# Kernel optimization log

Measured on AMD Instinct MI355X. Metric: run time of the kernel, lower is better.

## Reference

```python
import jax, jax.numpy as jnp
import numpy as np
import math

B, S, E, H = 4, 2048, 1024, 16
D = E // H
NEG_INF = -1e30  # stands in for -inf in masked_fill; softmax result identical for rows with valid entries


def setup_inputs() -> dict:
    key = jax.random.key(0)
    ks = jax.random.split(key, 7)
    sc = 1.0 / math.sqrt(E)
    return {
        "k": jax.random.normal(ks[0], (B, S, E), jnp.float32),
        "v": jax.random.normal(ks[1], (B, S, E), jnp.float32),
        "q": jax.random.normal(ks[2], (B, S, E), jnp.float32),
        "Wk": jax.random.normal(ks[3], (E, E), jnp.float32) * sc,
        "Wv": jax.random.normal(ks[4], (E, E), jnp.float32) * sc,
        "Wq": jax.random.normal(ks[5], (E, E), jnp.float32) * sc,
        "Wo": jax.random.normal(ks[6], (E, E), jnp.float32) * sc,
    }


def reference(k, v, q, Wk, Wv, Wq, Wo):
    # Linear(bias=False): y = x @ W.T
    kp = (k @ Wk.T).reshape(B, S, H, D).transpose(0, 2, 1, 3)  # [B,H,S,D]
    vp = (v @ Wv.T).reshape(B, S, H, D).transpose(0, 2, 1, 3)
    qp = (q @ Wq.T).reshape(B, S, H, D).transpose(0, 2, 1, 3)
    qp = qp / jnp.sqrt(jnp.asarray(D, qp.dtype))
    scores = jnp.einsum("bhqd,bhkd->bhqk", qp, kp)  # [B,H,S,S]
    causal = jnp.tril(jnp.ones((S, S), bool))  # [S,S]
    scores = jnp.where(causal[None, None], scores, NEG_INF)
    attn = jax.nn.softmax(scores, axis=-1)  # dropout p=0.0 (eval) -> identity
    out = jnp.einsum("bhqk,bhkd->bhqd", attn, vp)
    out = out.transpose(0, 2, 1, 3).reshape(B, S, E)
    return out @ Wo.T
```

## Files before the change

### kernel.cpp

```cpp
#include <hip/hip_runtime.h>

typedef __bf16 bf16_t;
typedef __bf16 bf16x8 __attribute__((ext_vector_type(8)));
typedef float f32x4 __attribute__((ext_vector_type(4)));
typedef float f32x16 __attribute__((ext_vector_type(16)));


__device__ __forceinline__ void async_copy16(const void* g, void* l) {
  __builtin_amdgcn_global_load_lds(
      (const __attribute__((address_space(1))) void*)g,
      (__attribute__((address_space(3))) void*)l, 16, 0, 0);
}

__device__ __forceinline__ unsigned pk_bf16(float lo, float hi) {
  unsigned r;
  asm("v_cvt_pk_bf16_f32 %0, %1, %2" : "=v"(r) : "v"(lo), "v"(hi));
  return r;
}

__global__ void cvt_all_kernel(const float* __restrict__ q, const float* __restrict__ k,
                               const float* __restrict__ v, const float* __restrict__ wk,
                               const float* __restrict__ wv, const float* __restrict__ wq,
                               const float* __restrict__ wo, uint2* __restrict__ out) {
  constexpr int QX = 2097152, QW = 262144;
  int g = blockIdx.x * 256 + threadIdx.x;
  const float* in; int off;
  if (g < QX)               { in = q;  off = 0; }
  else if (g < 2 * QX)      { in = k;  off = QX; }
  else if (g < 3 * QX)      { in = v;  off = 2 * QX; }
  else if (g < 3 * QX + QW)     { in = wk; off = 3 * QX; }
  else if (g < 3 * QX + 2 * QW) { in = wv; off = 3 * QX + QW; }
  else if (g < 3 * QX + 3 * QW) { in = wq; off = 3 * QX + 2 * QW; }
  else                          { in = wo; off = 3 * QX + 3 * QW; }
  float4 val = ((const float4*)in)[g - off];
  union { bf16_t h[4]; uint2 u; } cv;
  cv.h[0] = (bf16_t)val.x; cv.h[1] = (bf16_t)val.y;
  cv.h[2] = (bf16_t)val.z; cv.h[3] = (bf16_t)val.w;
  out[g] = cv.u;
}

__global__ __launch_bounds__(256) void qkv_kernel(
    const bf16_t* __restrict__ qb, const bf16_t* __restrict__ kb, const bf16_t* __restrict__ vb,
    const bf16_t* __restrict__ wqb, const bf16_t* __restrict__ wkb, const bf16_t* __restrict__ wvb,
    bf16_t* __restrict__ Qp, bf16_t* __restrict__ Kp, bf16_t* __restrict__ Vt, float qscale)
{
  constexpr int K = 1024;
  __shared__ __align__(16) bf16_t As[128 * 32];
  __shared__ __align__(16) bf16_t Bs[128 * 32];
  const int tid  = threadIdx.x;
  const int lane = tid & 63;
  const int wid  = tid >> 6;
  const int quad = lane >> 4;
  const int l16  = lane & 15;
  const int bx = blockIdx.x, by = blockIdx.y;
  const int sel = by >> 3, sub = by & 7;
  const bf16_t *X, *W; bf16_t* Y; float scale = 1.0f;
  int m0, n0;
  if (sel == 0)      { X = qb;  W = wqb; Y = Qp; m0 = bx * 128; n0 = sub * 128; scale = qscale; }
  else if (sel == 1) { X = kb;  W = wkb; Y = Kp; m0 = bx * 128; n0 = sub * 128; }
  else               { X = wvb; W = vb;  Y = Vt; m0 = sub * 128; n0 = bx * 128; }
  const int wm = (wid >> 1) * 64;
  const int wn = (wid & 1) * 64;
  const int swz = quad ^ ((l16 >> 1) & 3);

  f32x4 acc[4][4] = {};

  for (int k0 = 0; k0 < K; k0 += 32) {
#pragma unroll
    for (int p = 0; p < 2; ++p) {
      int c = tid + p * 256;
      int row = c >> 2;
      int seg = ((c & 3) ^ ((c >> 3) & 3)) * 8;
      async_copy16(&X[(size_t)(m0 + row) * K + k0 + seg], (char*)As + (p * 256 + wid * 64) * 16);
      async_copy16(&W[(size_t)(n0 + row) * K + k0 + seg], (char*)Bs + (p * 256 + wid * 64) * 16);
    }
    __syncthreads();
    bf16x8 af[4], bfr[4];
#pragma unroll
    for (int i = 0; i < 4; ++i)
      af[i] = *(const bf16x8*)((const char*)As + ((wm + i * 16 + l16) * 4 + swz) * 16);
#pragma unroll
    for (int j = 0; j < 4; ++j)
      bfr[j] = *(const bf16x8*)((const char*)Bs + ((wn + j * 16 + l16) * 4 + swz) * 16);
#pragma unroll
    for (int i = 0; i < 4; ++i)
#pragma unroll
      for (int j = 0; j < 4; ++j)
        acc[i][j] = __builtin_amdgcn_mfma_f32_16x16x32_bf16(af[i], bfr[j], acc[i][j], 0, 0, 0);
    __syncthreads();
  }

#pragma unroll
  for (int i = 0; i < 4; ++i)
#pragma unroll
    for (int j = 0; j < 4; ++j)
#pragma unroll
      for (int r = 0; r < 4; ++r) {
        int row = m0 + wm + i * 16 + quad * 4 + r;
        int col = n0 + wn + j * 16 + l16;
        float val = acc[i][j][r] * scale;
        if (sel < 2) {
          int b = row >> 11, s = row & 2047;
          int h = col >> 6,  d = col & 63;
          Y[(((size_t)(b * 16 + h) << 11) + s) * 64 + d] = (bf16_t)val;
        } else {
          int h = row >> 6,  d = row & 63;
          int b = col >> 11, s = col & 2047;
          Y[(((size_t)((b * 16 + h) * 64 + d)) << 11) + s] = (bf16_t)val;
        }
      }
}

__global__ __launch_bounds__(256) void out_gemm_kernel(
    const bf16_t* __restrict__ X, const bf16_t* __restrict__ W,
    float* __restrict__ Y, int M, int N, int K)
{
  __shared__ __align__(16) bf16_t As[128 * 32];
  __shared__ __align__(16) bf16_t Bs[128 * 32];
  const int tid  = threadIdx.x;
  const int lane = tid & 63;
  const int wid  = tid >> 6;
  const int quad = lane >> 4;
  const int l16  = lane & 15;
  const int m0 = blockIdx.x * 128;
  const int n0 = blockIdx.y * 128;
  const int wm = (wid >> 1) * 64;
  const int wn = (wid & 1) * 64;
  const int swz = quad ^ ((l16 >> 1) & 3);

  f32x4 acc[4][4] = {};

  for (int k0 = 0; k0 < K; k0 += 32) {
#pragma unroll
    for (int p = 0; p < 2; ++p) {
      int c = tid + p * 256;
      int row = c >> 2;
      int seg = ((c & 3) ^ ((c >> 3) & 3)) * 8;
      async_copy16(&X[(size_t)(m0 + row) * K + k0 + seg], (char*)As + (p * 256 + wid * 64) * 16);
      async_copy16(&W[(size_t)(n0 + row) * K + k0 + seg], (char*)Bs + (p * 256 + wid * 64) * 16);
    }
    __syncthreads();
    bf16x8 af[4], bfr[4];
#pragma unroll
    for (int i = 0; i < 4; ++i)
      af[i] = *(const bf16x8*)((const char*)As + ((wm + i * 16 + l16) * 4 + swz) * 16);
#pragma unroll
    for (int j = 0; j < 4; ++j)
      bfr[j] = *(const bf16x8*)((const char*)Bs + ((wn + j * 16 + l16) * 4 + swz) * 16);
#pragma unroll
    for (int i = 0; i < 4; ++i)
#pragma unroll
      for (int j = 0; j < 4; ++j)
        acc[i][j] = __builtin_amdgcn_mfma_f32_16x16x32_bf16(af[i], bfr[j], acc[i][j], 0, 0, 0);
    __syncthreads();
  }

#pragma unroll
  for (int i = 0; i < 4; ++i)
#pragma unroll
    for (int j = 0; j < 4; ++j)
#pragma unroll
      for (int r = 0; r < 4; ++r) {
        int row = m0 + wm + i * 16 + quad * 4 + r;
        int col = n0 + wn + j * 16 + l16;
        Y[(size_t)row * N + col] = acc[i][j][r];
      }
}

__global__ __launch_bounds__(256, 3) void attn_kernel(
    const bf16_t* __restrict__ Qp, const bf16_t* __restrict__ Kp,
    const bf16_t* __restrict__ Vt, bf16_t* __restrict__ O,
    float* __restrict__ Oacc, float* __restrict__ Racc)
{
  constexpr int S = 2048, D = 64, E = 1024;
  constexpr int BQ = 128, BK = 64;
  __shared__ __align__(16) bf16_t Ks[3][8 * 64 * 8];
  __shared__ __align__(16) bf16_t Vs[2][8 * 64 * 8];
  float* rsbuf = (float*)Ks;

  const int tid = threadIdx.x, lane = tid & 63, wid = tid >> 6;
  const int l31 = lane & 31, hi = lane >> 5;

  const signed char QT_TAB[24] = {15,15,7,14,14,13,13,6,12,12,11,11,5,10,10,9,9,4,8,8,3,2,1,0};
  const signed char HF_TAB[24] = {0,1,2,0,1,0,1,2,0,1,0,1,2,0,1,0,1,2,0,1,2,2,2,2};
  const int rank = (int)blockIdx.x >> 6;
  const int bh   = (int)blockIdx.x & 63;
  const int b = bh >> 4, h = bh & 15;
  const int qt = QT_TAB[rank];
  const int hf = HF_TAB[rank];
  const int nks = 2 * qt + 2;
  int s0, s1, half; bool direct;
  if (hf == 2) { s0 = 0; s1 = nks; half = 0; direct = true; }
  else         { half = hf; s0 = half ? nks / 2 : 0; s1 = half ? nks : nks / 2; direct = false; }

  const int q0 = qt * BQ;
  const size_t base  = (size_t)bh * S * D;
  const size_t baseV = (size_t)bh * D * S;
  const int qmin = q0 + wid * 32;
  const int qmax = qmin + 31;

  bf16x8 qf[4];
#pragma unroll
  for (int ks = 0; ks < 4; ++ks)
    qf[ks] = *(const bf16x8*)&Qp[base + (size_t)(qmin + l31) * D + ks * 16 + hi * 8];

  auto stageK = [&](int kt, int buf) {
#pragma unroll
    for (int is = 0; is < 2; ++is) {
      const int c = is * 256 + tid;
      const int p = c >> 6, row = c & 63;
      async_copy16(&Kp[base + (size_t)(kt * BK + row) * D + p * 8],
                   (char*)Ks[buf] + (is * 256 + wid * 64) * 16);
    }
  };
  auto stageV = [&](int kt, int buf) {
#pragma unroll
    for (int is = 0; is < 2; ++is) {
      const int c = is * 256 + tid;
      const int p = c >> 6, row = c & 63;
      async_copy16(&Vt[baseV + (size_t)row * S + kt * BK + p * 8],
                   (char*)Vs[buf] + (is * 256 + wid * 64) * 16);
    }
  };

  stageK(s0, s0 % 3);
  stageV(s0, s0 & 1);
  if (s0 + 1 < s1) stageK(s0 + 1, (s0 + 1) % 3);

  const f32x16 z16 = {};
  f32x16 oa0 = {}, oa1 = {};
  float rs = 0.0f;

  for (int kt = s0; kt < s1; ++kt) {
    const int k0 = kt * BK;
    const bool live = (k0 <= qmax);
    if (kt + 1 < s1) { asm volatile("s_waitcnt vmcnt(4)" ::: "memory"); }
    else             { asm volatile("s_waitcnt vmcnt(2)" ::: "memory"); }
    __builtin_amdgcn_s_barrier();
    __builtin_amdgcn_sched_barrier(0);
    if (kt + 1 < s1) stageV(kt + 1, (kt + 1) & 1);
    if (kt + 2 < s1) stageK(kt + 2, (kt + 2) % 3);

    unsigned pw[16];
    if (live) {
      const bf16_t* ksb = Ks[kt % 3];
      f32x16 sc0, sc1;
      {
        const bf16x8 kf0 = *(const bf16x8*)&ksb[(hi * 64 + l31) * 8];
        const bf16x8 kf1 = *(const bf16x8*)&ksb[(hi * 64 + 32 + l31) * 8];
        sc0 = __builtin_amdgcn_mfma_f32_32x32x16_bf16(kf0, qf[0], z16, 0, 0, 0);
        sc1 = __builtin_amdgcn_mfma_f32_32x32x16_bf16(kf1, qf[0], z16, 0, 0, 0);
      }
#pragma unroll
      for (int ks = 1; ks < 4; ++ks) {
        const bf16x8 kf0 = *(const bf16x8*)&ksb[((ks * 2 + hi) * 64 + l31) * 8];
        const bf16x8 kf1 = *(const bf16x8*)&ksb[((ks * 2 + hi) * 64 + 32 + l31) * 8];
        sc0 = __builtin_amdgcn_mfma_f32_32x32x16_bf16(kf0, qf[ks], sc0, 0, 0, 0);
        sc1 = __builtin_amdgcn_mfma_f32_32x32x16_bf16(kf1, qf[ks], sc1, 0, 0, 0);
      }
      if (k0 + 63 > qmin) {
        const int qg = qmin + l31;
#pragma unroll
        for (int r = 0; r < 16; ++r) {
          const int kg = k0 + (r & 3) + 8 * (r >> 2) + 4 * hi;
          if (kg > qg)      sc0[r] = -1e30f;
          if (kg + 32 > qg) sc1[r] = -1e30f;
        }
      }
#pragma unroll
      for (int r = 0; r < 16; ++r) {
        sc0[r] = __builtin_amdgcn_exp2f(sc0[r]);
        sc1[r] = __builtin_amdgcn_exp2f(sc1[r]);
      }
      {
        float s0a = 0.f, s1a = 0.f, s2a = 0.f, s3a = 0.f;
#pragma unroll
        for (int r = 0; r < 16; r += 4) {
          s0a += sc0[r]     + sc1[r];
          s1a += sc0[r + 1] + sc1[r + 1];
          s2a += sc0[r + 2] + sc1[r + 2];
          s3a += sc0[r + 3] + sc1[r + 3];
        }
        rs += (s0a + s1a) + (s2a + s3a);
      }
      {
        unsigned a0 = pk_bf16(sc0[0], sc0[1]),   a1 = pk_bf16(sc0[2], sc0[3]);
        unsigned b0 = pk_bf16(sc0[4], sc0[5]),   b1 = pk_bf16(sc0[6], sc0[7]);
        unsigned c0 = pk_bf16(sc0[8], sc0[9]),   c1 = pk_bf16(sc0[10], sc0[11]);
        unsigned d0 = pk_bf16(sc0[12], sc0[13]), d1 = pk_bf16(sc0[14], sc0[15]);
        asm("v_permlane32_swap_b32 %0, %1" : "+v"(a0), "+v"(b0));
        asm("v_permlane32_swap_b32 %0, %1" : "+v"(a1), "+v"(b1));
        asm("v_permlane32_swap_b32 %0, %1" : "+v"(c0), "+v"(d0));
        asm("v_permlane32_swap_b32 %0, %1" : "+v"(c1), "+v"(d1));
        pw[0] = a0; pw[1] = a1; pw[2] = b0; pw[3] = b1;
        pw[4] = c0; pw[5] = c1; pw[6] = d0; pw[7] = d1;
      }
      {
        unsigned a0 = pk_bf16(sc1[0], sc1[1]),   a1 = pk_bf16(sc1[2], sc1[3]);
        unsigned b0 = pk_bf16(sc1[4], sc1[5]),   b1 = pk_bf16(sc1[6], sc1[7]);
        unsigned c0 = pk_bf16(sc1[8], sc1[9]),   c1 = pk_bf16(sc1[10], sc1[11]);
        unsigned d0 = pk_bf16(sc1[12], sc1[13]), d1 = pk_bf16(sc1[14], sc1[15]);
        asm("v_permlane32_swap_b32 %0, %1" : "+v"(a0), "+v"(b0));
        asm("v_permlane32_swap_b32 %0, %1" : "+v"(a1), "+v"(b1));
        asm("v_permlane32_swap_b32 %0, %1" : "+v"(c0), "+v"(d0));
        asm("v_permlane32_swap_b32 %0, %1" : "+v"(c1), "+v"(d1));
        pw[8]  = a0; pw[9]  = a1; pw[10] = b0; pw[11] = b1;
        pw[12] = c0; pw[13] = c1; pw[14] = d0; pw[15] = d1;
      }
    }
    if (kt + 2 < s1)      { asm volatile("s_waitcnt vmcnt(6)" ::: "memory"); }
    else if (kt + 1 < s1) { asm volatile("s_waitcnt vmcnt(4)" ::: "memory"); }
    else                  { asm volatile("s_waitcnt vmcnt(0)" ::: "memory"); }
    __builtin_amdgcn_s_barrier();
    __builtin_amdgcn_sched_barrier(0);
    if (live) {
      const bf16_t* vsb = Vs[kt & 1];
      union U8 { unsigned u[4]; bf16x8 v; };
#pragma unroll
      for (int kb = 0; kb < 2; ++kb)
#pragma unroll
        for (int ks2 = 0; ks2 < 2; ++ks2) {
          U8 pu;
          pu.u[0] = pw[kb * 8 + ks2 * 4 + 0];
          pu.u[1] = pw[kb * 8 + ks2 * 4 + 1];
          pu.u[2] = pw[kb * 8 + ks2 * 4 + 2];
          pu.u[3] = pw[kb * 8 + ks2 * 4 + 3];
          const int pnl = kb * 4 + ks2 * 2 + hi;
          const bf16x8 vf0 = *(const bf16x8*)&vsb[(pnl * 64 + l31) * 8];
          const bf16x8 vf1 = *(const bf16x8*)&vsb[(pnl * 64 + 32 + l31) * 8];
          oa0 = __builtin_amdgcn_mfma_f32_32x32x16_bf16(pu.v, vf0, oa0, 0, 0, 0);
          oa1 = __builtin_amdgcn_mfma_f32_32x32x16_bf16(pu.v, vf1, oa1, 0, 0, 0);
        }
    }
  }

  const float full = rs + __shfl(rs, lane ^ 32);
  if (direct) {
    __syncthreads();
    if (lane < 32) rsbuf[wid * 32 + l31] = full;
    __syncthreads();
#pragma unroll
    for (int r = 0; r < 16; ++r) {
      const int crow = (r & 3) + 8 * (r >> 2) + 4 * hi;
      const float inv = __builtin_amdgcn_rcpf(rsbuf[wid * 32 + crow]);
      const int row = q0 + wid * 32 + crow;
      const size_t rowoff = ((size_t)(b * S + row)) * E + h * D;
      O[rowoff + l31]      = (bf16_t)(oa0[r] * inv);
      O[rowoff + 32 + l31] = (bf16_t)(oa1[r] * inv);
    }
  } else {
    float* Oh = Oacc + (size_t)half * (64 * 1024 * 64);
    float* Rh = Racc + (size_t)half * (64 * 1024);
    if (lane < 32) Rh[(size_t)bh * 1024 + (qmin + l31 - 1024)] = full;
#pragma unroll
    for (int r = 0; r < 16; ++r) {
      const int crow = (r & 3) + 8 * (r >> 2) + 4 * hi;
      const int row = q0 + wid * 32 + crow;
      float* dst = &Oh[((size_t)bh * 1024 + (row - 1024)) * 64];
      dst[l31]      = oa0[r];
      dst[32 + l31] = oa1[r];
    }
  }
}

__global__ void attn_norm_kernel(const float* __restrict__ Oacc,
                                 const float* __restrict__ Racc,
                                 bf16_t* __restrict__ O) {
  constexpr size_t OHALF = (size_t)64 * 1024 * 64;
  constexpr size_t RHALF = (size_t)64 * 1024;
  const int g = blockIdx.x * 256 + threadIdx.x;
  const int r = g >> 4;
  const int dq = (g & 15) * 4;
  const int bh = r >> 10, srow = r & 1023;
  const int b = bh >> 4, h = bh & 15;
  const float4 v0 = *(const float4*)&Oacc[(size_t)r * 64 + dq];
  const float4 v1 = *(const float4*)&Oacc[OHALF + (size_t)r * 64 + dq];
  const float inv = __builtin_amdgcn_rcpf(Racc[r] + Racc[RHALF + r]);
  union { bf16_t hh[4]; uint2 u; } cv;
  cv.hh[0] = (bf16_t)((v0.x + v1.x) * inv);
  cv.hh[1] = (bf16_t)((v0.y + v1.y) * inv);
  cv.hh[2] = (bf16_t)((v0.z + v1.z) * inv);
  cv.hh[3] = (bf16_t)((v0.w + v1.w) * inv);
  const size_t off = ((size_t)(b * 2048 + 1024 + srow)) * 1024 + h * 64 + dq;
  *(uint2*)&O[off] = cv.u;
}

extern "C" void kernel_launch(void* const* d_in, const int* in_sizes, int n_in,
                              void* d_out, int out_size, void* d_ws, size_t ws_size,
                              hipStream_t stream) {
  const float* k_in = (const float*)d_in[0];
  const float* v_in = (const float*)d_in[1];
  const float* q_in = (const float*)d_in[2];
  const float* Wk_in = (const float*)d_in[3];
  const float* Wv_in = (const float*)d_in[4];
  const float* Wq_in = (const float*)d_in[5];
  const float* Wo_in = (const float*)d_in[6];
  float* out = (float*)d_out;

  constexpr int    M = 8192, N = 1024, K = 1024;
  constexpr size_t SZ_X = (size_t)M * K * 2;
  constexpr size_t SZ_W = (size_t)N * K * 2;

  char* ws = (char*)d_ws;
  bf16_t* qb  = (bf16_t*)(ws);
  bf16_t* kb  = (bf16_t*)(ws + SZ_X);
  bf16_t* vb  = (bf16_t*)(ws + 2 * SZ_X);
  bf16_t* wkb = (bf16_t*)(ws + 3 * SZ_X);
  bf16_t* wvb = (bf16_t*)(ws + 3 * SZ_X + SZ_W);
  bf16_t* wqb = (bf16_t*)(ws + 3 * SZ_X + 2 * SZ_W);
  bf16_t* wob = (bf16_t*)(ws + 3 * SZ_X + 3 * SZ_W);
  bf16_t* Qp  = (bf16_t*)(ws + 3 * SZ_X + 4 * SZ_W);
  bf16_t* Kp  = (bf16_t*)(ws + 4 * SZ_X + 4 * SZ_W);
  bf16_t* Vtg = (bf16_t*)(ws + 5 * SZ_X + 4 * SZ_W);
  bf16_t* Ob  = qb;
  float* Oacc = (float*)(ws + SZ_X);
  float* Racc = (float*)(ws + 3 * SZ_X);

  cvt_all_kernel<<<28672, 256, 0, stream>>>(q_in, k_in, v_in, Wk_in, Wv_in, Wq_in, Wo_in,
                                            (uint2*)ws);

  qkv_kernel<<<dim3(64, 24), 256, 0, stream>>>(qb, kb, vb, wqb, wkb, wvb,
                                               Qp, Kp, Vtg, 0.125f * 1.44269504f);

  attn_kernel<<<dim3(1536), 256, 0, stream>>>(Qp, Kp, Vtg, Ob, Oacc, Racc);

  attn_norm_kernel<<<4096, 256, 0, stream>>>(Oacc, Racc, Ob);

  out_gemm_kernel<<<dim3(M / 128, N / 128), 256, 0, stream>>>(Ob, wob, out, M, N, K);
}
```

Measured before the change: 307.2 us.

## Triple-buffer async LDS loads in projection GEMMs and remap blocks for L2 locality

Both the QKV and output-projection GEMMs now keep three LDS buffers and prefetch two k-tiles ahead. Partial vmcnt waits plus one barrier per iteration replace the two __syncthreads per step, so global-to-LDS copies overlap MFMA work. The grids become 1D with a swizzled block index that groups 8 M-tiles with all N-tiles, aiming to improve L2 reuse of activation rows. The cost is three times the LDS per block (48KB) and a launch-bounds hint of 3 blocks per CU.

```diff
diff --git a/kernel.cpp b/kernel.cpp
--- a/kernel.cpp
+++ b/kernel.cpp
@@ -39,21 +39,24 @@
   out[g] = cv.u;
 }
 
-__global__ __launch_bounds__(256) void qkv_kernel(
+__global__ __launch_bounds__(256, 3) void qkv_kernel(
     const bf16_t* __restrict__ qb, const bf16_t* __restrict__ kb, const bf16_t* __restrict__ vb,
     const bf16_t* __restrict__ wqb, const bf16_t* __restrict__ wkb, const bf16_t* __restrict__ wvb,
     bf16_t* __restrict__ Qp, bf16_t* __restrict__ Kp, bf16_t* __restrict__ Vt, float qscale)
 {
-  constexpr int K = 1024;
-  __shared__ __align__(16) bf16_t As[128 * 32];
-  __shared__ __align__(16) bf16_t Bs[128 * 32];
+  constexpr int K = 1024, NKT = 32;
+  __shared__ __align__(16) bf16_t As[3][128 * 32];
+  __shared__ __align__(16) bf16_t Bs[3][128 * 32];
   const int tid  = threadIdx.x;
   const int lane = tid & 63;
   const int wid  = tid >> 6;
   const int quad = lane >> 4;
   const int l16  = lane & 15;
-  const int bx = blockIdx.x, by = blockIdx.y;
-  const int sel = by >> 3, sub = by & 7;
+  const int wg  = (int)blockIdx.x;
+  const int g   = (wg & 7) + ((wg >> 6) << 3);
+  const int sub = (wg >> 3) & 7;
+  const int sel = g >> 6;
+  const int bx  = g & 63;
   const bf16_t *X, *W; bf16_t* Y; float scale = 1.0f;
   int m0, n0;
   if (sel == 0)      { X = qb;  W = wqb; Y = Qp; m0 = bx * 128; n0 = sub * 128; scale = qscale; }
@@ -63,31 +66,46 @@
   const int wn = (wid & 1) * 64;
   const int swz = quad ^ ((l16 >> 1) & 3);
 
-  f32x4 acc[4][4] = {};
-
-  for (int k0 = 0; k0 < K; k0 += 32) {
+  auto stage = [&](int kt, int buf) {
+    const int k0 = kt * 32;
 #pragma unroll
     for (int p = 0; p < 2; ++p) {
       int c = tid + p * 256;
       int row = c >> 2;
       int seg = ((c & 3) ^ ((c >> 3) & 3)) * 8;
-      async_copy16(&X[(size_t)(m0 + row) * K + k0 + seg], (char*)As + (p * 256 + wid * 64) * 16);
-      async_copy16(&W[(size_t)(n0 + row) * K + k0 + seg], (char*)Bs + (p * 256 + wid * 64) * 16);
-    }
-    __syncthreads();
+      async_copy16(&X[(size_t)(m0 + row) * K + k0 + seg],
+                   (char*)As[buf] + (p * 256 + wid * 64) * 16);
+      async_copy16(&W[(size_t)(n0 + row) * K + k0 + seg],
+                   (char*)Bs[buf] + (p * 256 + wid * 64) * 16);
+    }
+  };
+
+  stage(0, 0);
+  stage(1, 1);
+
+  f32x4 acc[4][4] = {};
+
+  for (int kt = 0; kt < NKT; ++kt) {
+    if (kt + 1 < NKT) { asm volatile("s_waitcnt vmcnt(4)" ::: "memory"); }
+    else              { asm volatile("s_waitcnt vmcnt(0)" ::: "memory"); }
+    __builtin_amdgcn_s_barrier();
+    __builtin_amdgcn_sched_barrier(0);
+    if (kt + 2 < NKT) stage(kt + 2, (kt + 2) % 3);
+
+    const bf16_t* as = As[kt % 3];
+    const bf16_t* bs = Bs[kt % 3];
     bf16x8 af[4], bfr[4];
 #pragma unroll
     for (int i = 0; i < 4; ++i)
-      af[i] = *(const bf16x8*)((const char*)As + ((wm + i * 16 + l16) * 4 + swz) * 16);
+      af[i] = *(const bf16x8*)((const char*)as + ((wm + i * 16 + l16) * 4 + swz) * 16);
 #pragma unroll
     for (int j = 0; j < 4; ++j)
-      bfr[j] = *(const bf16x8*)((const char*)Bs + ((wn + j * 16 + l16) * 4 + swz) * 16);
+      bfr[j] = *(const bf16x8*)((const char*)bs + ((wn + j * 16 + l16) * 4 + swz) * 16);
 #pragma unroll
     for (int i = 0; i < 4; ++i)
 #pragma unroll
       for (int j = 0; j < 4; ++j)
         acc[i][j] = __builtin_amdgcn_mfma_f32_16x16x32_bf16(af[i], bfr[j], acc[i][j], 0, 0, 0);
-    __syncthreads();
   }
 
 #pragma unroll
@@ -111,48 +129,67 @@
       }
 }
 
-__global__ __launch_bounds__(256) void out_gemm_kernel(
+__global__ __launch_bounds__(256, 3) void out_gemm_kernel(
     const bf16_t* __restrict__ X, const bf16_t* __restrict__ W,
     float* __restrict__ Y, int M, int N, int K)
 {
-  __shared__ __align__(16) bf16_t As[128 * 32];
-  __shared__ __align__(16) bf16_t Bs[128 * 32];
+  constexpr int NKT = 32;
+  __shared__ __align__(16) bf16_t As[3][128 * 32];
+  __shared__ __align__(16) bf16_t Bs[3][128 * 32];
   const int tid  = threadIdx.x;
   const int lane = tid & 63;
   const int wid  = tid >> 6;
   const int quad = lane >> 4;
   const int l16  = lane & 15;
-  const int m0 = blockIdx.x * 128;
-  const int n0 = blockIdx.y * 128;
+  const int wg = (int)blockIdx.x;
+  const int bx = (wg & 7) + ((wg >> 6) << 3);
+  const int by = (wg >> 3) & 7;
+  const int m0 = bx * 128;
+  const int n0 = by * 128;
   const int wm = (wid >> 1) * 64;
   const int wn = (wid & 1) * 64;
   const int swz = quad ^ ((l16 >> 1) & 3);
 
-  f32x4 acc[4][4] = {};
-
-  for (int k0 = 0; k0 < K; k0 += 32) {
+  auto stage = [&](int kt, int buf) {
+    const int k0 = kt * 32;
 #pragma unroll
     for (int p = 0; p < 2; ++p) {
       int c = tid + p * 256;
       int row = c >> 2;
       int seg = ((c & 3) ^ ((c >> 3) & 3)) * 8;
-      async_copy16(&X[(size_t)(m0 + row) * K + k0 + seg], (char*)As + (p * 256 + wid * 64) * 16);
-      async_copy16(&W[(size_t)(n0 + row) * K + k0 + seg], (char*)Bs + (p * 256 + wid * 64) * 16);
-    }
-    __syncthreads();
+      async_copy16(&X[(size_t)(m0 + row) * K + k0 + seg],
+                   (char*)As[buf] + (p * 256 + wid * 64) * 16);
+      async_copy16(&W[(size_t)(n0 + row) * K + k0 + seg],
+                   (char*)Bs[buf] + (p * 256 + wid * 64) * 16);
+    }
+  };
+
+  stage(0, 0);
+  stage(1, 1);
+
+  f32x4 acc[4][4] = {};
+
+  for (int kt = 0; kt < NKT; ++kt) {
+    if (kt + 1 < NKT) { asm volatile("s_waitcnt vmcnt(4)" ::: "memory"); }
+    else              { asm volatile("s_waitcnt vmcnt(0)" ::: "memory"); }
+    __builtin_amdgcn_s_barrier();
+    __builtin_amdgcn_sched_barrier(0);
+    if (kt + 2 < NKT) stage(kt + 2, (kt + 2) % 3);
+
+    const bf16_t* as = As[kt % 3];
+    const bf16_t* bs = Bs[kt % 3];
     bf16x8 af[4], bfr[4];
 #pragma unroll
     for (int i = 0; i < 4; ++i)
-      af[i] = *(const bf16x8*)((const char*)As + ((wm + i * 16 + l16) * 4 + swz) * 16);
+      af[i] = *(const bf16x8*)((const char*)as + ((wm + i * 16 + l16) * 4 + swz) * 16);
 #pragma unroll
     for (int j = 0; j < 4; ++j)
-      bfr[j] = *(const bf16x8*)((const char*)Bs + ((wn + j * 16 + l16) * 4 + swz) * 16);
+      bfr[j] = *(const bf16x8*)((const char*)bs + ((wn + j * 16 + l16) * 4 + swz) * 16);
 #pragma unroll
     for (int i = 0; i < 4; ++i)
 #pragma unroll
       for (int j = 0; j < 4; ++j)
         acc[i][j] = __builtin_amdgcn_mfma_f32_16x16x32_bf16(af[i], bfr[j], acc[i][j], 0, 0, 0);
-    __syncthreads();
   }
 
 #pragma unroll
@@ -419,12 +456,12 @@
   cvt_all_kernel<<<28672, 256, 0, stream>>>(q_in, k_in, v_in, Wk_in, Wv_in, Wq_in, Wo_in,
                                             (uint2*)ws);
 
-  qkv_kernel<<<dim3(64, 24), 256, 0, stream>>>(qb, kb, vb, wqb, wkb, wvb,
-                                               Qp, Kp, Vtg, 0.125f * 1.44269504f);
+  qkv_kernel<<<dim3(1536), 256, 0, stream>>>(qb, kb, vb, wqb, wkb, wvb,
+                                             Qp, Kp, Vtg, 0.125f * 1.44269504f);
 
   attn_kernel<<<dim3(1536), 256, 0, stream>>>(Qp, Kp, Vtg, Ob, Oacc, Racc);
 
   attn_norm_kernel<<<4096, 256, 0, stream>>>(Oacc, Racc, Ob);
 
-  out_gemm_kernel<<<dim3(M / 128, N / 128), 256, 0, stream>>>(Ob, wob, out, M, N, K);
-}
+  out_gemm_kernel<<<dim3(512), 256, 0, stream>>>(Ob, wob, out, M, N, K);
+}
```

Result: faster. 299.6 us (-2.5%).

## Triple-buffer output GEMM loads and remap blocks for L2 locality

Applied to the files above, without the earlier changes.

The output projection GEMM moves from a single-buffered load/sync/compute loop to a three-stage async pipeline. It waits with vmcnt and issues one barrier per k-tile, so global-to-LDS copies overlap the MFMA work. The grid is flattened to 1D and block indices are remapped into 8x8 tile groups to improve L2 reuse of X and W. The loop now hardcodes K/32=32 tiles and assumes M=8192, N=1024, and it triples LDS use.

```diff
diff --git a/kernel.cpp b/kernel.cpp
--- a/kernel.cpp
+++ b/kernel.cpp
@@ -111,48 +111,67 @@
       }
 }
 
-__global__ __launch_bounds__(256) void out_gemm_kernel(
+__global__ __launch_bounds__(256, 3) void out_gemm_kernel(
     const bf16_t* __restrict__ X, const bf16_t* __restrict__ W,
     float* __restrict__ Y, int M, int N, int K)
 {
-  __shared__ __align__(16) bf16_t As[128 * 32];
-  __shared__ __align__(16) bf16_t Bs[128 * 32];
+  constexpr int NKT = 32;
+  __shared__ __align__(16) bf16_t As[3][128 * 32];
+  __shared__ __align__(16) bf16_t Bs[3][128 * 32];
   const int tid  = threadIdx.x;
   const int lane = tid & 63;
   const int wid  = tid >> 6;
   const int quad = lane >> 4;
   const int l16  = lane & 15;
-  const int m0 = blockIdx.x * 128;
-  const int n0 = blockIdx.y * 128;
+  const int wg = (int)blockIdx.x;
+  const int bx = (wg & 7) + ((wg >> 6) << 3);
+  const int by = (wg >> 3) & 7;
+  const int m0 = bx * 128;
+  const int n0 = by * 128;
   const int wm = (wid >> 1) * 64;
   const int wn = (wid & 1) * 64;
   const int swz = quad ^ ((l16 >> 1) & 3);
 
-  f32x4 acc[4][4] = {};
-
-  for (int k0 = 0; k0 < K; k0 += 32) {
+  auto stage = [&](int kt, int buf) {
+    const int k0 = kt * 32;
 #pragma unroll
     for (int p = 0; p < 2; ++p) {
       int c = tid + p * 256;
       int row = c >> 2;
       int seg = ((c & 3) ^ ((c >> 3) & 3)) * 8;
-      async_copy16(&X[(size_t)(m0 + row) * K + k0 + seg], (char*)As + (p * 256 + wid * 64) * 16);
-      async_copy16(&W[(size_t)(n0 + row) * K + k0 + seg], (char*)Bs + (p * 256 + wid * 64) * 16);
-    }
-    __syncthreads();
+      async_copy16(&X[(size_t)(m0 + row) * K + k0 + seg],
+                   (char*)As[buf] + (p * 256 + wid * 64) * 16);
+      async_copy16(&W[(size_t)(n0 + row) * K + k0 + seg],
+                   (char*)Bs[buf] + (p * 256 + wid * 64) * 16);
+    }
+  };
+
+  stage(0, 0);
+  stage(1, 1);
+
+  f32x4 acc[4][4] = {};
+
+  for (int kt = 0; kt < NKT; ++kt) {
+    if (kt + 1 < NKT) { asm volatile("s_waitcnt vmcnt(4)" ::: "memory"); }
+    else              { asm volatile("s_waitcnt vmcnt(0)" ::: "memory"); }
+    __builtin_amdgcn_s_barrier();
+    __builtin_amdgcn_sched_barrier(0);
+    if (kt + 2 < NKT) stage(kt + 2, (kt + 2) % 3);
+
+    const bf16_t* as = As[kt % 3];
+    const bf16_t* bs = Bs[kt % 3];
     bf16x8 af[4], bfr[4];
 #pragma unroll
     for (int i = 0; i < 4; ++i)
-      af[i] = *(const bf16x8*)((const char*)As + ((wm + i * 16 + l16) * 4 + swz) * 16);
+      af[i] = *(const bf16x8*)((const char*)as + ((wm + i * 16 + l16) * 4 + swz) * 16);
 #pragma unroll
     for (int j = 0; j < 4; ++j)
-      bfr[j] = *(const bf16x8*)((const char*)Bs + ((wn + j * 16 + l16) * 4 + swz) * 16);
+      bfr[j] = *(const bf16x8*)((const char*)bs + ((wn + j * 16 + l16) * 4 + swz) * 16);
 #pragma unroll
     for (int i = 0; i < 4; ++i)
 #pragma unroll
       for (int j = 0; j < 4; ++j)
         acc[i][j] = __builtin_amdgcn_mfma_f32_16x16x32_bf16(af[i], bfr[j], acc[i][j], 0, 0, 0);
-    __syncthreads();
   }
 
 #pragma unroll
@@ -426,5 +445,5 @@
 
   attn_norm_kernel<<<4096, 256, 0, stream>>>(Oacc, Racc, Ob);
 
-  out_gemm_kernel<<<dim3(M / 128, N / 128), 256, 0, stream>>>(Ob, wob, out, M, N, K);
-}
+  out_gemm_kernel<<<dim3(512), 256, 0, stream>>>(Ob, wob, out, M, N, K);
+}
```

After: 302.6 us. No clear change (-1.5%).
